# Optimization experiments

Measured on AMD Instinct MI355X. Metric: run time of the kernel, lower is better.

## Reference

```python
import jax, jax.numpy as jnp
import numpy as np

B, D_MODEL, SSM = 2, 96, 2
D_INNER = SSM * D_MODEL          # 192
D_STATE = 16
DT_RANK = 6                      # ceil(96/16)
K = 2
H = W = 64
L = H * W


def leaky(x):
    return jnp.where(x > 0, x, 0.2 * x)


def conv2d(x, w, b, pad):
    y = jax.lax.conv_general_dilated(x, w, (1, 1), [(pad, pad), (pad, pad)],
                                     dimension_numbers=('NCHW', 'OIHW', 'NCHW'))
    return y + b[None, :, None, None]


def pos_encoding(h, w, d):
    # Faithful to torch: emb_x||emb_y has width 2*d, then truncated to d (only emb_x survives).
    ys = jnp.arange(h, dtype=jnp.float32) / (h - 1)
    xs = jnp.arange(w, dtype=jnp.float32) / (w - 1)
    gy, gx = jnp.meshgrid(ys, xs, indexing='ij')
    dim_each = d // 2
    inv_freq = 1.0 / (10000.0 ** (jnp.arange(dim_each, dtype=jnp.float32) / dim_each))
    px = gx[..., None] * inv_freq
    py = gy[..., None] * inv_freq
    emb = jnp.concatenate([jnp.sin(px), jnp.cos(px), jnp.sin(py), jnp.cos(py)], axis=-1)
    return emb.reshape(h * w, -1)[:, :d]  # [L, d]


def selective_scan(u, delta, A, Bs, Cs, Dp):
    # u, delta: [B,K,C,L]; A: [K,C,N]; Bs, Cs: [B,K,N,L]; Dp: [K,C]
    dT = jnp.moveaxis(delta, -1, 0)
    uT = jnp.moveaxis(u, -1, 0)
    BT = jnp.moveaxis(Bs, -1, 0)
    CT = jnp.moveaxis(Cs, -1, 0)
    h0 = jnp.zeros(u.shape[:3] + (A.shape[-1],), u.dtype)  # [B,K,C,N]

    def step(h, inp):
        dt, ut, bt, ct = inp
        h = h * jnp.exp(dt[..., None] * A) + (dt * ut)[..., None] * bt[:, :, None, :]
        return h, jnp.einsum('bkcn,bkn->bkc', h, ct)

    _, ys = jax.lax.scan(step, h0, (dT, uT, BT, CT))
    return jnp.moveaxis(ys, 0, -1) + Dp[None, :, :, None] * u  # [B,K,C,L]


def _branch(x, order, pe_map, x_proj_w, dt_w, dt_b, A_log, Dp, depth_proj, depth_sig):
    # x: [B,C,H,W]; order: [B,L] permutation; pe_map: [C,L]
    Bn, C = x.shape[0], x.shape[1]
    x_flat = x.reshape(Bn, C, L)
    x_sorted = jnp.take_along_axis(x_flat, order[:, None, :], axis=2)       # [B,C,L]
    xs = jnp.stack([x_sorted, x_sorted[:, :, ::-1]], axis=1)                # [B,2,C,L]
    pe = jnp.take_along_axis(jnp.broadcast_to(pe_map[None], (Bn, C, L)), order[:, None, :], axis=2)
    xs = xs + jnp.stack([pe, pe[:, :, ::-1]], axis=1)

    x_dbl = jnp.einsum('bkdl,kcd->bkcl', xs, x_proj_w)                      # [B,2,R+2N,L]
    dts_r = x_dbl[:, :, :DT_RANK]
    B_orig = x_dbl[:, :, DT_RANK:DT_RANK + D_STATE]
    C_orig = x_dbl[:, :, DT_RANK + D_STATE:]

    orders2 = jnp.stack([order, order[:, ::-1]], axis=1)                    # [B,2,L]
    dproj = jnp.take_along_axis(depth_proj, orders2[:, :, None, :], axis=3) # [B,2,2N,L]
    B_depth, C_depth = dproj[:, :, :D_STATE], dproj[:, :, D_STATE:]
    wgt = jnp.take_along_axis(jnp.broadcast_to(depth_sig[:, None], (Bn, 2, D_STATE, L)),
                              orders2[:, :, None, :], axis=3)
    Bs = (1 - wgt) * B_orig + wgt * B_depth
    Cs = (1 - wgt) * C_orig + wgt * C_depth

    delta = jax.nn.softplus(jnp.einsum('bkrl,kdr->bkdl', dts_r, dt_w) + dt_b[None, :, :, None])
    A = -jnp.exp(A_log.reshape(K, C, D_STATE))
    y = selective_scan(xs, delta, A, Bs, Cs, Dp.reshape(K, C))              # [B,2,C,L]

    inv = jnp.argsort(order, axis=-1)                                       # undo the scan order
    y_fwd = jnp.take_along_axis(y[:, 0], inv[:, None, :], axis=2)
    y_bwd = jnp.take_along_axis(y[:, 1, :, ::-1], inv[:, None, :], axis=2)
    return y_fwd + y_bwd                                                    # [B,C,L]


def _layernorm(x, g, b):
    mu = x.mean(-1, keepdims=True)
    var = ((x - mu) ** 2).mean(-1, keepdims=True)
    return (x - mu) * jax.lax.rsqrt(var + 1e-5) * g + b


def setup_inputs() -> dict:
    key = jax.random.key(0)
    ks = jax.random.split(key, 16)
    s = 0.02
    A_log = jnp.tile(jnp.log(jnp.arange(1, D_STATE + 1, dtype=jnp.float32))[None], (K * D_INNER, 1))
    return {
        'x_T': jax.random.normal(ks[0], (B, D_INNER, H, W), jnp.float32),
        'x_R': jax.random.normal(ks[1], (B, D_INNER, H, W), jnp.float32),
        'proximity_map': jax.random.uniform(ks[2], (B, D_INNER, H, W), jnp.float32),
        'fuse_w': jax.random.normal(ks[3], (1, 2 * D_INNER, 3, 3), jnp.float32) * s,
        'fuse_b': jnp.zeros((1,), jnp.float32),
        'x_proj_w': jax.random.normal(ks[4], (K, DT_RANK + 2 * D_STATE, D_INNER), jnp.float32) * s,
        'dt_w': jax.random.normal(ks[5], (K, D_INNER, DT_RANK), jnp.float32) * s,
        'dt_b': jax.random.uniform(ks[6], (K, D_INNER), jnp.float32, -4.0, -2.0),
        'A_log_T': A_log, 'A_log_R': A_log,
        'D_T': jnp.ones((K * D_INNER,), jnp.float32),
        'D_R': jnp.ones((K * D_INNER,), jnp.float32),
        'depth_enc_w': jax.random.normal(ks[7], (D_INNER, D_INNER, 1, 1), jnp.float32) * s,
        'depth_enc_b': jnp.zeros((D_INNER,), jnp.float32),
        'depth_proj_w': jax.random.normal(ks[8], (K, 2 * D_STATE, D_INNER), jnp.float32) * s,
        'sig_w': jax.random.normal(ks[9], (D_STATE, D_INNER, 1, 1), jnp.float32) * s,
        'sig_b': jnp.zeros((D_STATE,), jnp.float32),
        'ln_g': jnp.ones((D_INNER,), jnp.float32),
        'ln_b': jnp.zeros((D_INNER,), jnp.float32),
    }


def reference(x_T, x_R, proximity_map, fuse_w, fuse_b, x_proj_w, dt_w, dt_b,
              A_log_T, A_log_R, D_T, D_R, depth_enc_w, depth_enc_b,
              depth_proj_w, sig_w, sig_b, ln_g, ln_b):
    # depth-conditioned proximity maps -> scan orders
    pm_T = jax.nn.sigmoid(leaky(conv2d(jnp.concatenate([x_T, proximity_map], 1), fuse_w, fuse_b, 1)))
    pm_R = jax.nn.sigmoid(leaky(conv2d(jnp.concatenate([x_R, proximity_map], 1), fuse_w, fuse_b, 1)))
    # T: depth-aware regional scan (near-to-far: descending); R: global scan (ascending)
    order_T = jnp.argsort(-pm_T.reshape(B, L), axis=-1)
    order_R = jnp.argsort(pm_R.reshape(B, L), axis=-1)

    pe_map = pos_encoding(H, W, D_INNER).T                                  # [C,L]
    depth_feat = leaky(conv2d(proximity_map, depth_enc_w, depth_enc_b, 0)).reshape(B, D_INNER, L)
    depth_proj = jnp.einsum('bdl,kcd->bkcl', depth_feat, depth_proj_w)      # [B,K,2N,L]
    depth_sig = jax.nn.sigmoid(leaky(conv2d(proximity_map, sig_w, sig_b, 0))).reshape(B, D_STATE, L)

    y_T = _branch(x_T, order_T, pe_map, x_proj_w, dt_w, dt_b, A_log_T, D_T, depth_proj, depth_sig)
    y_R = _branch(x_R, order_R, pe_map, x_proj_w, dt_w, dt_b, A_log_R, D_R, depth_proj, depth_sig)

    y_T = _layernorm(y_T.transpose(0, 2, 1), ln_g, ln_b).reshape(B, H, W, D_INNER)
    y_R = _layernorm(y_R.transpose(0, 2, 1), ln_g, ln_b).reshape(B, H, W, D_INNER)
    return jnp.stack([y_T, y_R])  # [2,B,H,W,C]
```

## Files before the change

kernel.cpp:

```cpp
#include <hip/hip_runtime.h>
#include <hip/hip_bf16.h>
#include <math.h>

#define BATCH 2
#define DI 192
#define NST 16
#define DTR 6
#define KK 2
#define LL 4096
#define CT 512
#define NCK (LL/CT)

__global__ __launch_bounds__(256) void prep_kernel(
        float* __restrict__ pe,
        const float* __restrict__ wde, const float* __restrict__ dpw,
        const float* __restrict__ sgw, float* __restrict__ wtT,
        const float* __restrict__ xT, const float* __restrict__ xR,
        const float* __restrict__ prox, const float* __restrict__ fw,
        float* __restrict__ pbuf) {
    __shared__ float wl[288];
    __shared__ float red[2][4][64];
    int bid = blockIdx.x;
    int tid = threadIdx.x;
    if (bid < 48) {
        int i = bid * 256 + tid;
        if (i >= 64 * DI) return;
        int col = i / DI, c = i % DI;
        float gx = (float)col / 63.f;
        int m = (c < 96) ? c : (c - 96);
        float invf = expf(-(float)m * (logf(10000.f) / 96.f));
        float ang = gx * invf;
        pe[i] = (c < 96) ? sinf(ang) : cosf(ang);
        return;
    }
    if (bid < 252) {
        int idx = (bid - 48) * 256 + tid;
        if (idx < 192 * 272) {
            int i = idx / 272, j = idx % 272;
            float v;
            if (j < 192) v = wde[j * DI + i];
            else if (j < 256) v = dpw[(j - 192) * DI + i];
            else v = sgw[(j - 256) * DI + i];
            wtT[idx] = v;
        }
        return;
    }
    int fid = bid - 252;
    int cg = fid >> 7;
    int rem = fid & 127;
    int row = rem >> 1;
    int b = rem & 1;
    if (tid < 288) {
        int cl = (tid % 144) / 9, tap = tid % 9;
        int half = tid / 144;
        wl[tid] = fw[(half * DI + cg * 16 + cl) * 9 + tap];
    }
    __syncthreads();
    int px = tid & 63, g = tid >> 6;
    float aT = 0.f, aR = 0.f, aP = 0.f;
    #pragma unroll
    for (int cc = 0; cc < 4; ++cc) {
        int cl = g * 4 + cc;
        int c = cg * 16 + cl;
        const float* xTb = xT + (size_t)(b * DI + c) * LL;
        const float* xRb = xR + (size_t)(b * DI + c) * LL;
        const float* pb  = prox + (size_t)(b * DI + c) * LL;
        const float* wT = wl + cl * 9;
        const float* wP = wl + 144 + cl * 9;
        #pragma unroll
        for (int ky = 0; ky < 3; ++ky) {
            int yy = row + ky - 1;
            if (yy < 0 || yy > 63) continue;
            #pragma unroll
            for (int kx = 0; kx < 3; ++kx) {
                int xx = px + kx - 1;
                bool in = (xx >= 0 && xx < 64);
                int o = yy * 64 + (in ? xx : 0);
                float mT = in ? xTb[o] : 0.f;
                float mR = in ? xRb[o] : 0.f;
                float mP = in ? pb[o] : 0.f;
                float wTv = wT[ky * 3 + kx], wPv = wP[ky * 3 + kx];
                aT += mT * wTv;
                aR += mR * wTv;
                aP += mP * wPv;
            }
        }
    }
    red[0][g][px] = aT + aP;
    red[1][g][px] = aR + aP;
    __syncthreads();
    if (tid < 128) {
        int X = tid >> 6, x = tid & 63;
        float s = red[X][0][x] + red[X][1][x] + red[X][2][x] + red[X][3][x];
        pbuf[(size_t)(cg * 4 + X * 2 + b) * LL + row * 64 + x] = s;
    }
}

union MidSmem {
    struct { unsigned int keys[LL]; int cnts[4][64]; } srt;
    struct { float pvs[8][DI]; float dfs[8][DI]; } dep;
    struct { float tile[32][33]; } trp;
};

__global__ __launch_bounds__(256) void mid_kernel(
        const float* __restrict__ pbuf, const float* __restrict__ fb,
        int* __restrict__ ord,
        const float* __restrict__ prox, const float* __restrict__ wtT,
        const float* __restrict__ bde, const float* __restrict__ sgb,
        float* __restrict__ dproj, float* __restrict__ dsig,
        const float* __restrict__ xT, const float* __restrict__ xR,
        float* __restrict__ xpeT, float* __restrict__ xpeR,
        const float* __restrict__ pe) {
    __shared__ MidSmem sm;
    int bid = blockIdx.x;
    int tid = threadIdx.x;
    if (bid < 256) {
        int eblk = bid & 63;
        int Xb = bid >> 6;
        int X = Xb >> 1;
        float bias = fb[0];
        for (int i = tid; i < LL; i += 256) {
            float v = bias;
            #pragma unroll
            for (int cg = 0; cg < 12; ++cg)
                v += pbuf[(size_t)(cg * 4 + Xb) * LL + i];
            if (X == 0) v = -v;
            int bits = __float_as_int(v);
            sm.srt.keys[i] = (bits < 0) ? ~(unsigned)bits : ((unsigned)bits | 0x80000000u);
        }
        __syncthreads();
        int el = tid & 63;
        int q = tid >> 6;
        int e = eblk * 64 + el;
        unsigned ui = sm.srt.keys[e];
        int count = 0;
        int j0 = q * (LL / 4);
        #pragma unroll 4
        for (int j = j0; j < j0 + LL / 4; ++j) {
            unsigned uj = sm.srt.keys[j];
            count += (uj < ui) || (uj == ui && j < e);
        }
        sm.srt.cnts[q][el] = count;
        __syncthreads();
        if (tid < 64) {
            int rank = sm.srt.cnts[0][tid] + sm.srt.cnts[1][tid] +
                       sm.srt.cnts[2][tid] + sm.srt.cnts[3][tid];
            int i = eblk * 64 + tid;
            ord[(size_t)Xb * LL + rank] = i;
        }
        return;
    }
    if (bid < 1280) {
        int bl0 = (bid - 256) * 8;
        int b = bl0 >> 12;
        int l0 = bl0 & 4095;
        for (int t = tid; t < 8 * DI; t += 256) {
            int i = t >> 3, l = t & 7;
            sm.dep.pvs[l][i] = prox[((size_t)b * DI + i) * LL + l0 + l];
        }
        __syncthreads();
        if (tid < DI) {
            float acc[8];
            #pragma unroll
            for (int l = 0; l < 8; ++l) acc[l] = 0.f;
            const float* wp = wtT + tid;
            for (int i = 0; i < DI; ++i) {
                float w = wp[i * 272];
                #pragma unroll
                for (int l = 0; l < 8; ++l) acc[l] += w * sm.dep.pvs[l][i];
            }
            float bias = bde[tid];
            #pragma unroll
            for (int l = 0; l < 8; ++l) {
                float v = acc[l] + bias;
                sm.dep.dfs[l][tid] = (v > 0.f) ? v : 0.2f * v;
            }
        }
        __syncthreads();
        if (tid < 160) {
            int o = tid >> 1;
            int ph = (tid & 1) * 4;
            float acc[4] = {0.f, 0.f, 0.f, 0.f};
            const float* wp = wtT + 192 + o;
            for (int i = 0; i < DI; ++i) {
                float w = wp[i * 272];
                #pragma unroll
                for (int p = 0; p < 4; ++p) acc[p] += w * sm.dep.dfs[ph + p][i];
            }
            if (o < 64) {
                #pragma unroll
                for (int p = 0; p < 4; ++p)
                    dproj[(size_t)(bl0 + ph + p) * 64 + o] = acc[p];
            } else {
                float bias = sgb[o - 64];
                #pragma unroll
                for (int p = 0; p < 4; ++p) {
                    float v = acc[p] + bias;
                    v = (v > 0.f) ? v : 0.2f * v;
                    dsig[(size_t)(bl0 + ph + p) * NST + (o - 64)] = 1.f / (1.f + __expf(-v));
                }
            }
        }
        return;
    }
    {
        int tbid = bid - 1280;
        int lx = tbid & 127;
        int cy = (tbid >> 7) % 6;
        int z = tbid / 768;
        int which = z >> 1;
        int b = z & 1;
        const float* in = which ? xR : xT;
        float* out = which ? xpeR : xpeT;
        int l0 = lx * 32, c0 = cy * 32;
        int tx = tid & 31, ty = tid >> 5;
        #pragma unroll
        for (int r = 0; r < 4; ++r) {
            int c = c0 + ty + r * 8;
            sm.trp.tile[ty + r * 8][tx] = in[(size_t)(b * DI + c) * LL + l0 + tx];
        }
        __syncthreads();
        #pragma unroll
        for (int r = 0; r < 4; ++r) {
            int l = l0 + ty + r * 8;
            int c = c0 + tx;
            float v = sm.trp.tile[tx][ty + r * 8] + pe[(l & 63) * DI + c];
            out[(size_t)(b * LL + l) * DI + c] = v;
        }
    }
}

__global__ __launch_bounds__(512) void project_kernel(
        const float* __restrict__ xpeT, const float* __restrict__ xpeR,
        const int* __restrict__ ord,
        const float* __restrict__ xpw, const float* __restrict__ dtw,
        const float* __restrict__ dtb, const float* __restrict__ dproj,
        const float* __restrict__ dsig, float* __restrict__ dtb2,
        float* __restrict__ dub2, float* __restrict__ bscs2) {
    __shared__ float u[32][196];
    __shared__ float dbl[32][40];
    __shared__ int jarr[32];
    int id = blockIdx.x;
    int chunk = id & 127;
    int k = (id >> 7) & 1;
    int b = (id >> 8) & 1;
    int X = id >> 9;
    const float* xpe = X ? xpeR : xpeT;
    int R = (X * 2 + b) * 2 + k;
    int s0 = chunk * 32;
    int tid = threadIdx.x;
    if (tid < 32) {
        int s = s0 + tid;
        jarr[tid] = ord[(size_t)(X * 2 + b) * LL + ((k == 0) ? s : (LL - 1 - s))];
    }
    __syncthreads();
    for (int t = tid; t < 32 * 48; t += 512) {
        int l = t / 48, i4 = t % 48;
        *(float4*)&u[l][i4 * 4] =
            *(const float4*)(xpe + (size_t)(b * LL + jarr[l]) * DI + i4 * 4);
    }
    __syncthreads();
    {
        int og = tid >> 5, sl = tid & 31;
        const float* w0 = xpw + (size_t)(k * 38 + og) * DI;
        const float* w1 = w0 + 16 * DI;
        const float* w2 = w0 + 32 * DI;
        bool has2 = (og < 6);
        float a0 = 0.f, a1 = 0.f, a2 = 0.f;
        for (int i4 = 0; i4 < 48; ++i4) {
            float4 u4 = *(const float4*)&u[sl][i4 * 4];
            float4 x0 = *(const float4*)(w0 + i4 * 4);
            float4 x1 = *(const float4*)(w1 + i4 * 4);
            a0 += x0.x * u4.x + x0.y * u4.y + x0.z * u4.z + x0.w * u4.w;
            a1 += x1.x * u4.x + x1.y * u4.y + x1.z * u4.z + x1.w * u4.w;
            if (has2) {
                float4 x2 = *(const float4*)(w2 + i4 * 4);
                a2 += x2.x * u4.x + x2.y * u4.y + x2.z * u4.z + x2.w * u4.w;
            }
        }
        dbl[sl][og] = a0;
        dbl[sl][og + 16] = a1;
        if (has2) dbl[sl][og + 32] = a2;
    }
    __syncthreads();
    if (tid < 384) {
        int c = tid % 192;
        int h = tid / 192;
        float w[6];
        #pragma unroll
        for (int r = 0; r < 6; ++r) w[r] = dtw[(k * DI + c) * DTR + r];
        float bias = dtb[k * DI + c];
        float dtl[16], dul[16];
        #pragma unroll
        for (int sl = 0; sl < 16; ++sl) {
            int s = h * 16 + sl;
            float d = bias;
            #pragma unroll
            for (int r = 0; r < 6; ++r) d += w[r] * dbl[s][r];
            float sp = fmaxf(d, 0.f) + __logf(1.f + __expf(-fabsf(d)));
            dtl[sl] = sp;
            dul[sl] = sp * u[s][c];
        }
        size_t base = (size_t)(R * DI + c) * LL + s0 + h * 16;
        #pragma unroll
        for (int g = 0; g < 4; ++g) {
            *(float4*)(dtb2 + base + g * 4) =
                make_float4(dtl[g*4], dtl[g*4+1], dtl[g*4+2], dtl[g*4+3]);
            *(float4*)(dub2 + base + g * 4) =
                make_float4(dul[g*4], dul[g*4+1], dul[g*4+2], dul[g*4+3]);
        }
    }
    {
        int n = tid >> 5, sl = tid & 31;
        int j = jarr[sl];
        float wv = dsig[(size_t)(b * LL + j) * NST + n];
        float Bo = dbl[sl][6 + n], Co = dbl[sl][22 + n];
        float Bd = dproj[(size_t)(b * LL + j) * 64 + k * 32 + n];
        float Cd = dproj[(size_t)(b * LL + j) * 64 + k * 32 + 16 + n];
        size_t sb = (size_t)(R * 32 + n) * LL + s0 + sl;
        bscs2[sb] = (1.f - wv) * Bo + wv * Bd;
        bscs2[sb + (size_t)16 * LL] = (1.f - wv) * Co + wv * Cd;
    }
}

__global__ __launch_bounds__(512, 6) void scan_fused_kernel(
        const float* __restrict__ dtb2, const float* __restrict__ dub2,
        const float* __restrict__ bscs2, const float* __restrict__ AlogT,
        const float* __restrict__ AlogR, float* __restrict__ y) {
    __shared__ float ypart[2][8][CT + 4];
    int id = blockIdx.x;
    int c = id % DI;
    int bkx = id / DI;
    int X = bkx >> 2;
    int k = bkx & 1;
    const float* Alog = X ? AlogR : AlogT;
    int w = threadIdx.x >> 6;
    int t = threadIdx.x & 63;
    float A0 = -__expf(Alog[(k * DI + c) * NST + w]);
    float A1 = -__expf(Alog[(k * DI + c) * NST + w + 8]);
    size_t rowc = (size_t)(bkx * DI + c) * LL;
    const float* dtp = dtb2 + rowc;
    const float* dup = dub2 + rowc;
    const float* b0p = bscs2 + (size_t)(bkx * 32 + w) * LL;
    const float* c0p = b0p + (size_t)16 * LL;
    const float* b1p = b0p + (size_t)8 * LL;
    const float* c1p = c0p + (size_t)8 * LL;
    float* yrow = y + rowc;
    float Hc0 = 0.f, Hc1 = 0.f;
    int off = t * 8;
    for (int ck = 0; ck < NCK; ++ck) {
        int base = ck * CT;
        int o = base + off;
        float4 dA = *(const float4*)(dtp + o), dB = *(const float4*)(dtp + o + 4);
        float4 uA = *(const float4*)(dup + o), uB = *(const float4*)(dup + o + 4);
        float4 B0a = *(const float4*)(b0p + o), B0b = *(const float4*)(b0p + o + 4);
        float4 B1a = *(const float4*)(b1p + o), B1b = *(const float4*)(b1p + o + 4);
        float d[8]  = {dA.x, dA.y, dA.z, dA.w, dB.x, dB.y, dB.z, dB.w};
        float uu[8] = {uA.x, uA.y, uA.z, uA.w, uB.x, uB.y, uB.z, uB.w};
        float Bb0[8] = {B0a.x, B0a.y, B0a.z, B0a.w, B0b.x, B0b.y, B0b.z, B0b.w};
        float Bb1[8] = {B1a.x, B1a.y, B1a.z, B1a.w, B1b.x, B1b.y, B1b.z, B1b.w};
        float e0[8], e1[8], z0[8], z1[8];
        float S = 0.f, cb0 = 0.f, cb1 = 0.f;
        #pragma unroll
        for (int j = 0; j < 8; ++j) {
            e0[j] = __expf(d[j] * A0);
            e1[j] = __expf(d[j] * A1);
            z0[j] = uu[j] * Bb0[j];
            z1[j] = uu[j] * Bb1[j];
            S += d[j];
            cb0 = cb0 * e0[j] + z0[j];
            cb1 = cb1 * e1[j] + z1[j];
        }
        #pragma unroll
        for (int m = 1; m < 64; m <<= 1) {
            float sS = __shfl_up(S, m);
            float s0 = __shfl_up(cb0, m);
            float s1 = __shfl_up(cb1, m);
            if (t >= m) {
                cb0 += __expf(A0 * S) * s0;
                cb1 += __expf(A1 * S) * s1;
                S += sS;
            }
        }
        float Sf  = __shfl(S, 63);
        float b0f = __shfl(cb0, 63);
        float b1f = __shfl(cb1, 63);
        float Se  = __shfl_up(S, 1);
        float b0e = __shfl_up(cb0, 1);
        float b1e = __shfl_up(cb1, 1);
        if (t == 0) { Se = 0.f; b0e = 0.f; b1e = 0.f; }
        float h0 = __expf(A0 * Se) * Hc0 + b0e;
        float h1 = __expf(A1 * Se) * Hc1 + b1e;
        float nHc0 = __expf(A0 * Sf) * Hc0 + b0f;
        float nHc1 = __expf(A1 * Sf) * Hc1 + b1f;
        Hc0 = nHc0; Hc1 = nHc1;
        float4 C0a = *(const float4*)(c0p + o), C0b = *(const float4*)(c0p + o + 4);
        float4 C1a = *(const float4*)(c1p + o), C1b = *(const float4*)(c1p + o + 4);
        float Cc0[8] = {C0a.x, C0a.y, C0a.z, C0a.w, C0b.x, C0b.y, C0b.z, C0b.w};
        float Cc1[8] = {C1a.x, C1a.y, C1a.z, C1a.w, C1b.x, C1b.y, C1b.z, C1b.w};
        float yv[8];
        #pragma unroll
        for (int j = 0; j < 8; ++j) {
            h0 = h0 * e0[j] + z0[j];
            h1 = h1 * e1[j] + z1[j];
            yv[j] = h0 * Cc0[j] + h1 * Cc1[j];
        }
        *(float4*)&ypart[ck & 1][w][off] = make_float4(yv[0], yv[1], yv[2], yv[3]);
        *(float4*)&ypart[ck & 1][w][off + 4] = make_float4(yv[4], yv[5], yv[6], yv[7]);
        __syncthreads();
        if (threadIdx.x < 128) {
            int t4 = threadIdx.x * 4;
            float4 s = *(const float4*)&ypart[ck & 1][0][t4];
            #pragma unroll
            for (int r = 1; r < 8; ++r) {
                float4 v = *(const float4*)&ypart[ck & 1][r][t4];
                s.x += v.x; s.y += v.y; s.z += v.z; s.w += v.w;
            }
            *(float4*)(yrow + base + t4) = s;
        }
    }
}

__global__ __launch_bounds__(256) void ln_kernel(const float* __restrict__ y,
                          const float* __restrict__ xpeT, const float* __restrict__ xpeR,
                          const int* __restrict__ ord, const float* __restrict__ DvT,
                          const float* __restrict__ DvR, const float* __restrict__ g,
                          const float* __restrict__ beta, float* __restrict__ out) {
    __shared__ float y0t[DI][17];
    __shared__ float y1t[DI][17];
    int id = blockIdx.x;
    int X = id >> 9;
    int b = (id >> 8) & 1;
    int s0 = (id & 255) * 16;
    const float* xpe = X ? xpeR : xpeT;
    const float* Dvec = X ? DvR : DvT;
    int R0 = (X * 2 + b) * 2;
    int tid = threadIdx.x;
    for (int idx = tid; idx < DI * 16; idx += 256) {
        int c = idx >> 4, j = idx & 15;
        y0t[c][j] = y[((size_t)(R0 + 0) * DI + c) * LL + s0 + j];
        y1t[c][j] = y[((size_t)(R0 + 1) * DI + c) * LL + (LL - 1 - s0 - j)];
    }
    __syncthreads();
    int w = tid >> 6, lane = tid & 63;
    #pragma unroll
    for (int it = 0; it < 4; ++it) {
        int j = it * 4 + w;
        int l = ord[(size_t)(X * 2 + b) * LL + s0 + j];
        const float* xr = xpe + (size_t)(b * LL + l) * DI;
        float v[3];
        float sum = 0.f, sq = 0.f;
        #pragma unroll
        for (int r = 0; r < 3; ++r) {
            int c = lane + r * 64;
            float t = y0t[c][j] + y1t[c][j] + (Dvec[c] + Dvec[DI + c]) * xr[c];
            v[r] = t; sum += t; sq += t * t;
        }
        #pragma unroll
        for (int m = 1; m < 64; m <<= 1) {
            sum += __shfl_xor(sum, m);
            sq += __shfl_xor(sq, m);
        }
        float mu = sum * (1.f / 192.f);
        float var = sq * (1.f / 192.f) - mu * mu;
        float rs = rsqrtf(var + 1e-5f);
        float* op = out + ((size_t)(X * 2 + b) * LL + l) * DI;
        #pragma unroll
        for (int r = 0; r < 3; ++r) {
            int c = lane + r * 64;
            op[c] = (v[r] - mu) * rs * g[c] + beta[c];
        }
    }
}

extern "C" void kernel_launch(void* const* d_in, const int* in_sizes, int n_in,
                              void* d_out, int out_size, void* d_ws, size_t ws_size,
                              hipStream_t stream) {
    const float* x_T = (const float*)d_in[0];
    const float* x_R = (const float*)d_in[1];
    const float* prox = (const float*)d_in[2];
    const float* fuse_w = (const float*)d_in[3];
    const float* fuse_b = (const float*)d_in[4];
    const float* x_proj_w = (const float*)d_in[5];
    const float* dt_w = (const float*)d_in[6];
    const float* dt_b = (const float*)d_in[7];
    const float* A_log_T = (const float*)d_in[8];
    const float* A_log_R = (const float*)d_in[9];
    const float* D_T = (const float*)d_in[10];
    const float* D_R = (const float*)d_in[11];
    const float* depth_enc_w = (const float*)d_in[12];
    const float* depth_enc_b = (const float*)d_in[13];
    const float* depth_proj_w = (const float*)d_in[14];
    const float* sig_w = (const float*)d_in[15];
    const float* sig_b = (const float*)d_in[16];
    const float* ln_g = (const float*)d_in[17];
    const float* ln_b = (const float*)d_in[18];
    float* out = (float*)d_out;
    char* ws = (char*)d_ws;

    float* pe    = (float*)(ws + 0);
    int*   ord   = (int*)(ws + 114688);
    float* xpeR  = (float*)(ws + 245760);
    float* dproj = (float*)(ws + 6537216);
    float* dsig  = (float*)(ws + 8634368);
    float* xpeT  = (float*)(ws + 9158656);
    float* dtb2  = (float*)(ws + 15450112);
    float* dub2  = (float*)(ws + 40615936);
    float* bscs2 = (float*)(ws + 65781760);
    float* ybuf  = (float*)(ws + 69976064);
    float* pbuf  = dtb2;
    float* wtT   = bscs2;

    prep_kernel<<<1788, 256, 0, stream>>>(pe, depth_enc_w, depth_proj_w, sig_w, wtT,
                                          x_T, x_R, prox, fuse_w, pbuf);
    mid_kernel<<<4352, 256, 0, stream>>>(pbuf, fuse_b, ord, prox, wtT,
                                         depth_enc_b, sig_b, dproj, dsig,
                                         x_T, x_R, xpeT, xpeR, pe);
    project_kernel<<<1024, 512, 0, stream>>>(xpeT, xpeR, ord, x_proj_w, dt_w, dt_b,
                                             dproj, dsig, dtb2, dub2, bscs2);
    scan_fused_kernel<<<8 * DI, 512, 0, stream>>>(dtb2, dub2, bscs2, A_log_T, A_log_R, ybuf);
    ln_kernel<<<1024, 256, 0, stream>>>(ybuf, xpeT, xpeR, ord, D_T, D_R, ln_g, ln_b, out);
}
```

Measured before the change: 177.9 us.

## Process four state channels per wave in scan with 256-thread blocks

The scan kernel now runs with 4 waves per block instead of 8, each wave handling 4 state channels instead of 2. dt and u loads are shared across more channels, and the cross-wave shared-memory reduction shrinks from 8 to 4 partial rows. Per-step exp and B values are no longer cached in arrays but recomputed and reloaded in the second pass, which cuts register pressure at the cost of extra exp work and extra B loads. Each block does twice as much work per thread with half the threads.

After: 202.0 us. 13.5% more time.

```diff
diff --git a/kernel.cpp b/kernel.cpp
--- a/kernel.cpp
+++ b/kernel.cpp
@@ -323,11 +323,11 @@
     }
 }
 
-__global__ __launch_bounds__(512, 6) void scan_fused_kernel(
+__global__ __launch_bounds__(256) void scan_fused_kernel(
         const float* __restrict__ dtb2, const float* __restrict__ dub2,
         const float* __restrict__ bscs2, const float* __restrict__ AlogT,
         const float* __restrict__ AlogR, float* __restrict__ y) {
-    __shared__ float ypart[2][8][CT + 4];
+    __shared__ float ypart[2][4][CT + 4];
     int id = blockIdx.x;
     int c = id % DI;
     int bkx = id / DI;
@@ -336,74 +336,87 @@
     const float* Alog = X ? AlogR : AlogT;
     int w = threadIdx.x >> 6;
     int t = threadIdx.x & 63;
-    float A0 = -__expf(Alog[(k * DI + c) * NST + w]);
-    float A1 = -__expf(Alog[(k * DI + c) * NST + w + 8]);
+    float A[4];
+    #pragma unroll
+    for (int q = 0; q < 4; ++q)
+        A[q] = -__expf(Alog[(k * DI + c) * NST + (w + 4 * q)]);
     size_t rowc = (size_t)(bkx * DI + c) * LL;
     const float* dtp = dtb2 + rowc;
     const float* dup = dub2 + rowc;
-    const float* b0p = bscs2 + (size_t)(bkx * 32 + w) * LL;
-    const float* c0p = b0p + (size_t)16 * LL;
-    const float* b1p = b0p + (size_t)8 * LL;
-    const float* c1p = c0p + (size_t)8 * LL;
+    const float* bp = bscs2 + (size_t)(bkx * 32 + w) * LL;
+    const float* cp = bp + (size_t)16 * LL;
     float* yrow = y + rowc;
-    float Hc0 = 0.f, Hc1 = 0.f;
+    float Hc[4] = {0.f, 0.f, 0.f, 0.f};
     int off = t * 8;
     for (int ck = 0; ck < NCK; ++ck) {
-        int base = ck * CT;
-        int o = base + off;
+        int o = ck * CT + off;
         float4 dA = *(const float4*)(dtp + o), dB = *(const float4*)(dtp + o + 4);
+        float d[8] = {dA.x, dA.y, dA.z, dA.w, dB.x, dB.y, dB.z, dB.w};
         float4 uA = *(const float4*)(dup + o), uB = *(const float4*)(dup + o + 4);
-        float4 B0a = *(const float4*)(b0p + o), B0b = *(const float4*)(b0p + o + 4);
-        float4 B1a = *(const float4*)(b1p + o), B1b = *(const float4*)(b1p + o + 4);
-        float d[8]  = {dA.x, dA.y, dA.z, dA.w, dB.x, dB.y, dB.z, dB.w};
         float uu[8] = {uA.x, uA.y, uA.z, uA.w, uB.x, uB.y, uB.z, uB.w};
-        float Bb0[8] = {B0a.x, B0a.y, B0a.z, B0a.w, B0b.x, B0b.y, B0b.z, B0b.w};
-        float Bb1[8] = {B1a.x, B1a.y, B1a.z, B1a.w, B1b.x, B1b.y, B1b.z, B1b.w};
-        float e0[8], e1[8], z0[8], z1[8];
-        float S = 0.f, cb0 = 0.f, cb1 = 0.f;
-        #pragma unroll
-        for (int j = 0; j < 8; ++j) {
-            e0[j] = __expf(d[j] * A0);
-            e1[j] = __expf(d[j] * A1);
-            z0[j] = uu[j] * Bb0[j];
-            z1[j] = uu[j] * Bb1[j];
-            S += d[j];
-            cb0 = cb0 * e0[j] + z0[j];
-            cb1 = cb1 * e1[j] + z1[j];
+        float S = d[0] + d[1] + d[2] + d[3] + d[4] + d[5] + d[6] + d[7];
+        float cb[4];
+        #pragma unroll
+        for (int q = 0; q < 4; ++q) {
+            const float* bq = bp + (size_t)(4 * q) * LL;
+            float4 Ba = *(const float4*)(bq + o);
+            float4 Bb4 = *(const float4*)(bq + o + 4);
+            float acc = 0.f;
+            acc = acc * __expf(d[0] * A[q]) + uu[0] * Ba.x;
+            acc = acc * __expf(d[1] * A[q]) + uu[1] * Ba.y;
+            acc = acc * __expf(d[2] * A[q]) + uu[2] * Ba.z;
+            acc = acc * __expf(d[3] * A[q]) + uu[3] * Ba.w;
+            acc = acc * __expf(d[4] * A[q]) + uu[4] * Bb4.x;
+            acc = acc * __expf(d[5] * A[q]) + uu[5] * Bb4.y;
+            acc = acc * __expf(d[6] * A[q]) + uu[6] * Bb4.z;
+            acc = acc * __expf(d[7] * A[q]) + uu[7] * Bb4.w;
+            cb[q] = acc;
         }
         #pragma unroll
         for (int m = 1; m < 64; m <<= 1) {
             float sS = __shfl_up(S, m);
-            float s0 = __shfl_up(cb0, m);
-            float s1 = __shfl_up(cb1, m);
+            float s0 = __shfl_up(cb[0], m);
+            float s1 = __shfl_up(cb[1], m);
+            float s2 = __shfl_up(cb[2], m);
+            float s3 = __shfl_up(cb[3], m);
             if (t >= m) {
-                cb0 += __expf(A0 * S) * s0;
-                cb1 += __expf(A1 * S) * s1;
+                cb[0] += __expf(A[0] * S) * s0;
+                cb[1] += __expf(A[1] * S) * s1;
+                cb[2] += __expf(A[2] * S) * s2;
+                cb[3] += __expf(A[3] * S) * s3;
                 S += sS;
             }
         }
-        float Sf  = __shfl(S, 63);
-        float b0f = __shfl(cb0, 63);
-        float b1f = __shfl(cb1, 63);
-        float Se  = __shfl_up(S, 1);
-        float b0e = __shfl_up(cb0, 1);
-        float b1e = __shfl_up(cb1, 1);
-        if (t == 0) { Se = 0.f; b0e = 0.f; b1e = 0.f; }
-        float h0 = __expf(A0 * Se) * Hc0 + b0e;
-        float h1 = __expf(A1 * Se) * Hc1 + b1e;
-        float nHc0 = __expf(A0 * Sf) * Hc0 + b0f;
-        float nHc1 = __expf(A1 * Sf) * Hc1 + b1f;
-        Hc0 = nHc0; Hc1 = nHc1;
-        float4 C0a = *(const float4*)(c0p + o), C0b = *(const float4*)(c0p + o + 4);
-        float4 C1a = *(const float4*)(c1p + o), C1b = *(const float4*)(c1p + o + 4);
-        float Cc0[8] = {C0a.x, C0a.y, C0a.z, C0a.w, C0b.x, C0b.y, C0b.z, C0b.w};
-        float Cc1[8] = {C1a.x, C1a.y, C1a.z, C1a.w, C1b.x, C1b.y, C1b.z, C1b.w};
-        float yv[8];
-        #pragma unroll
-        for (int j = 0; j < 8; ++j) {
-            h0 = h0 * e0[j] + z0[j];
-            h1 = h1 * e1[j] + z1[j];
-            yv[j] = h0 * Cc0[j] + h1 * Cc1[j];
+        float Sf = __shfl(S, 63);
+        float Se = __shfl_up(S, 1);
+        if (t == 0) Se = 0.f;
+        float h[4];
+        #pragma unroll
+        for (int q = 0; q < 4; ++q) {
+            float bf = __shfl(cb[q], 63);
+            float be = __shfl_up(cb[q], 1);
+            if (t == 0) be = 0.f;
+            h[q] = __expf(A[q] * Se) * Hc[q] + be;
+            Hc[q] = __expf(A[q] * Sf) * Hc[q] + bf;
+        }
+        float yv[8] = {0.f, 0.f, 0.f, 0.f, 0.f, 0.f, 0.f, 0.f};
+        #pragma unroll
+        for (int q = 0; q < 4; ++q) {
+            const float* bq = bp + (size_t)(4 * q) * LL;
+            const float* cq = cp + (size_t)(4 * q) * LL;
+            float4 Ba = *(const float4*)(bq + o);
+            float4 Bb4 = *(const float4*)(bq + o + 4);
+            float4 Ca = *(const float4*)(cq + o);
+            float4 Cb4 = *(const float4*)(cq + o + 4);
+            float hq = h[q];
+            hq = hq * __expf(d[0] * A[q]) + uu[0] * Ba.x;  yv[0] += hq * Ca.x;
+            hq = hq * __expf(d[1] * A[q]) + uu[1] * Ba.y;  yv[1] += hq * Ca.y;
+            hq = hq * __expf(d[2] * A[q]) + uu[2] * Ba.z;  yv[2] += hq * Ca.z;
+            hq = hq * __expf(d[3] * A[q]) + uu[3] * Ba.w;  yv[3] += hq * Ca.w;
+            hq = hq * __expf(d[4] * A[q]) + uu[4] * Bb4.x; yv[4] += hq * Cb4.x;
+            hq = hq * __expf(d[5] * A[q]) + uu[5] * Bb4.y; yv[5] += hq * Cb4.y;
+            hq = hq * __expf(d[6] * A[q]) + uu[6] * Bb4.z; yv[6] += hq * Cb4.z;
+            hq = hq * __expf(d[7] * A[q]) + uu[7] * Bb4.w; yv[7] += hq * Cb4.w;
         }
         *(float4*)&ypart[ck & 1][w][off] = make_float4(yv[0], yv[1], yv[2], yv[3]);
         *(float4*)&ypart[ck & 1][w][off + 4] = make_float4(yv[4], yv[5], yv[6], yv[7]);
@@ -412,11 +425,11 @@
             int t4 = threadIdx.x * 4;
             float4 s = *(const float4*)&ypart[ck & 1][0][t4];
             #pragma unroll
-            for (int r = 1; r < 8; ++r) {
+            for (int r = 1; r < 4; ++r) {
                 float4 v = *(const float4*)&ypart[ck & 1][r][t4];
                 s.x += v.x; s.y += v.y; s.z += v.z; s.w += v.w;
             }
-            *(float4*)(yrow + base + t4) = s;
+            *(float4*)(yrow + ck * CT + t4) = s;
         }
     }
 }
@@ -518,6 +531,6 @@
                                          x_T, x_R, xpeT, xpeR, pe);
     project_kernel<<<1024, 512, 0, stream>>>(xpeT, xpeR, ord, x_proj_w, dt_w, dt_b,
                                              dproj, dsig, dtb2, dub2, bscs2);
-    scan_fused_kernel<<<8 * DI, 512, 0, stream>>>(dtb2, dub2, bscs2, A_log_T, A_log_R, ybuf);
+    scan_fused_kernel<<<8 * DI, 256, 0, stream>>>(dtb2, dub2, bscs2, A_log_T, A_log_R, ybuf);
     ln_kernel<<<1024, 256, 0, stream>>>(ybuf, xpeT, xpeR, ord, D_T, D_R, ln_g, ln_b, out);
 }
```

## Process two channels per scan block to reuse B/C loads

Applied to the files above, without the earlier changes.

Each scan block now handles two adjacent channels instead of one, halving the grid to 768 blocks. The B and C state rows, shared across channels, are loaded once per chunk and reused from cache for the second channel. The reduction step now sums both channels and adds a second barrier per chunk. The occupancy hint in the launch bounds is dropped, and there are fewer blocks than before to spread over the compute units.

Result: no change. 178.0 us (+0.1%).

```diff
diff --git a/kernel.cpp b/kernel.cpp
--- a/kernel.cpp
+++ b/kernel.cpp
@@ -323,34 +323,37 @@
     }
 }
 
-__global__ __launch_bounds__(512, 6) void scan_fused_kernel(
+__global__ __launch_bounds__(512) void scan_fused_kernel(
         const float* __restrict__ dtb2, const float* __restrict__ dub2,
         const float* __restrict__ bscs2, const float* __restrict__ AlogT,
         const float* __restrict__ AlogR, float* __restrict__ y) {
     __shared__ float ypart[2][8][CT + 4];
     int id = blockIdx.x;
-    int c = id % DI;
-    int bkx = id / DI;
+    int cp = id % 96;
+    int bkx = id / 96;
     int X = bkx >> 2;
     int k = bkx & 1;
     const float* Alog = X ? AlogR : AlogT;
     int w = threadIdx.x >> 6;
     int t = threadIdx.x & 63;
-    float A0 = -__expf(Alog[(k * DI + c) * NST + w]);
-    float A1 = -__expf(Alog[(k * DI + c) * NST + w + 8]);
-    size_t rowc = (size_t)(bkx * DI + c) * LL;
-    const float* dtp = dtb2 + rowc;
-    const float* dup = dub2 + rowc;
+    int c0 = cp * 2;
+    float A0_0 = -__expf(Alog[(k * DI + c0) * NST + w]);
+    float A1_0 = -__expf(Alog[(k * DI + c0) * NST + w + 8]);
+    float A0_1 = -__expf(Alog[(k * DI + c0 + 1) * NST + w]);
+    float A1_1 = -__expf(Alog[(k * DI + c0 + 1) * NST + w + 8]);
     const float* b0p = bscs2 + (size_t)(bkx * 32 + w) * LL;
     const float* c0p = b0p + (size_t)16 * LL;
     const float* b1p = b0p + (size_t)8 * LL;
     const float* c1p = c0p + (size_t)8 * LL;
-    float* yrow = y + rowc;
-    float Hc0 = 0.f, Hc1 = 0.f;
+    size_t rc0 = (size_t)(bkx * DI + c0) * LL;
+    size_t rc1 = rc0 + LL;
+    float Hc00 = 0.f, Hc10 = 0.f;
+    float Hc01 = 0.f, Hc11 = 0.f;
     int off = t * 8;
-    for (int ck = 0; ck < NCK; ++ck) {
-        int base = ck * CT;
-        int o = base + off;
+    int o = off;
+
+    auto chan = [&](float A0, float A1, const float* dtp, const float* dup,
+                    float& rHc0, float& rHc1, float (*yp)[CT + 4]) {
         float4 dA = *(const float4*)(dtp + o), dB = *(const float4*)(dtp + o + 4);
         float4 uA = *(const float4*)(dup + o), uB = *(const float4*)(dup + o + 4);
         float4 B0a = *(const float4*)(b0p + o), B0b = *(const float4*)(b0p + o + 4);
@@ -389,11 +392,11 @@
         float b0e = __shfl_up(cb0, 1);
         float b1e = __shfl_up(cb1, 1);
         if (t == 0) { Se = 0.f; b0e = 0.f; b1e = 0.f; }
-        float h0 = __expf(A0 * Se) * Hc0 + b0e;
-        float h1 = __expf(A1 * Se) * Hc1 + b1e;
-        float nHc0 = __expf(A0 * Sf) * Hc0 + b0f;
-        float nHc1 = __expf(A1 * Sf) * Hc1 + b1f;
-        Hc0 = nHc0; Hc1 = nHc1;
+        float h0 = __expf(A0 * Se) * rHc0 + b0e;
+        float h1 = __expf(A1 * Se) * rHc1 + b1e;
+        float nHc0 = __expf(A0 * Sf) * rHc0 + b0f;
+        float nHc1 = __expf(A1 * Sf) * rHc1 + b1f;
+        rHc0 = nHc0; rHc1 = nHc1;
         float4 C0a = *(const float4*)(c0p + o), C0b = *(const float4*)(c0p + o + 4);
         float4 C1a = *(const float4*)(c1p + o), C1b = *(const float4*)(c1p + o + 4);
         float Cc0[8] = {C0a.x, C0a.y, C0a.z, C0a.w, C0b.x, C0b.y, C0b.z, C0b.w};
@@ -405,19 +408,32 @@
             h1 = h1 * e1[j] + z1[j];
             yv[j] = h0 * Cc0[j] + h1 * Cc1[j];
         }
-        *(float4*)&ypart[ck & 1][w][off] = make_float4(yv[0], yv[1], yv[2], yv[3]);
-        *(float4*)&ypart[ck & 1][w][off + 4] = make_float4(yv[4], yv[5], yv[6], yv[7]);
-        __syncthreads();
-        if (threadIdx.x < 128) {
-            int t4 = threadIdx.x * 4;
-            float4 s = *(const float4*)&ypart[ck & 1][0][t4];
+        *(float4*)&yp[w][off] = make_float4(yv[0], yv[1], yv[2], yv[3]);
+        *(float4*)&yp[w][off + 4] = make_float4(yv[4], yv[5], yv[6], yv[7]);
+    };
+
+    for (int ck = 0; ck < NCK; ++ck) {
+        int base = ck * CT;
+        o = base + off;
+        {
+            chan(A0_0, A1_0, dtb2 + rc0, dub2 + rc0, Hc00, Hc10, ypart[0]);
+        }
+        {
+            chan(A0_1, A1_1, dtb2 + rc1, dub2 + rc1, Hc01, Hc11, ypart[1]);
+        }
+        __syncthreads();
+        if (threadIdx.x < 256) {
+            int ch = threadIdx.x >> 7;
+            int t4 = (threadIdx.x & 127) * 4;
+            float4 s = *(const float4*)&ypart[ch][0][t4];
             #pragma unroll
             for (int r = 1; r < 8; ++r) {
-                float4 v = *(const float4*)&ypart[ck & 1][r][t4];
+                float4 v = *(const float4*)&ypart[ch][r][t4];
                 s.x += v.x; s.y += v.y; s.z += v.z; s.w += v.w;
             }
-            *(float4*)(yrow + base + t4) = s;
-        }
+            *(float4*)(y + (ch ? rc1 : rc0) + base + t4) = s;
+        }
+        __syncthreads();
     }
 }
 
@@ -518,6 +534,6 @@
                                          x_T, x_R, xpeT, xpeR, pe);
     project_kernel<<<1024, 512, 0, stream>>>(xpeT, xpeR, ord, x_proj_w, dt_w, dt_b,
                                              dproj, dsig, dtb2, dub2, bscs2);
-    scan_fused_kernel<<<8 * DI, 512, 0, stream>>>(dtb2, dub2, bscs2, A_log_T, A_log_R, ybuf);
+    scan_fused_kernel<<<768, 512, 0, stream>>>(dtb2, dub2, bscs2, A_log_T, A_log_R, ybuf);
     ln_kernel<<<1024, 256, 0, stream>>>(ybuf, xpeT, xpeR, ord, D_T, D_R, ln_g, ln_b, out);
 }
```
